# Optimization experiments

Measured on AMD Instinct MI355X. Metric: run time of the kernel, lower is better.

## Reference

```python
import jax, jax.numpy as jnp
import numpy as np

B, L, D, F_, H = 64, 64, 512, 32, 512  # batch, seq_len, in_dim, fanout, hidden_dim


def setup_inputs() -> dict:
    key = jax.random.key(0)
    ks = jax.random.split(key, 8)
    x = jax.random.normal(ks[0], (B, L, D), dtype=jnp.float32)
    idx1 = jax.random.randint(ks[1], (B, F_), 0, L)          # hop-1 neighbor token ids
    idx2 = jax.random.randint(ks[2], (B, F_ * F_), 0, L)     # hop-2 neighbor token ids
    s_d = 1.0 / np.sqrt(D)
    s_h = 1.0 / np.sqrt(H)
    W_aggr0 = jax.random.normal(ks[3], (D, H), dtype=jnp.float32) * s_d
    b_aggr0 = jnp.zeros((H,), dtype=jnp.float32)
    W_self0 = jax.random.normal(ks[4], (D, H), dtype=jnp.float32) * s_d
    W_aggr1 = jax.random.normal(ks[5], (H, H), dtype=jnp.float32) * s_h
    b_aggr1 = jnp.zeros((H,), dtype=jnp.float32)
    W_self1 = jax.random.normal(ks[6], (H, H), dtype=jnp.float32) * s_h
    return {"x": x, "idx1": idx1, "idx2": idx2,
            "W_aggr0": W_aggr0, "b_aggr0": b_aggr0, "W_self0": W_self0,
            "W_aggr1": W_aggr1, "b_aggr1": b_aggr1, "W_self1": W_self1}


def _sage_gcn(src, nbr, W_aggr, b_aggr, W_self):
    # src: [B, N, d]; nbr: [B, N, F, d]. mean-aggregate + linear, sum with self-transform.
    aggr = jnp.mean(nbr, axis=2) @ W_aggr + b_aggr          # NeighborAggregator('mean')
    return src @ W_self + aggr                               # aggr_hidden_method='sum'


def reference(x, idx1, idx2, W_aggr0, b_aggr0, W_self0, W_aggr1, b_aggr1, W_self1):
    # Gather sampled node features per aspect (level 0 = aspect node itself, index 0).
    f0 = x[:, :1, :]                                               # [B, 1, D]
    f1 = jnp.take_along_axis(x, idx1[:, :, None], axis=1)          # [B, F, D]
    f2 = jnp.take_along_axis(x, idx2[:, :, None], axis=1)          # [B, F*F, D]

    # Layer 0 (shared gcn[0] weights across hops), leaky_relu activation.
    h0 = jax.nn.leaky_relu(_sage_gcn(f0, f1[:, None, :, :], W_aggr0, b_aggr0, W_self0))          # [B,1,H]
    h1 = jax.nn.leaky_relu(_sage_gcn(f1, f2.reshape(B, F_, F_, D), W_aggr0, b_aggr0, W_self0))   # [B,F,H]

    # Layer 1 (gcn[-1], activation=None).
    out = _sage_gcn(h0, h1[:, None, :, :], W_aggr1, b_aggr1, W_self1)                             # [B,1,H]
    return out
```

## Files before the change

kernel.cpp:

```cpp
#include <hip/hip_runtime.h>
#include <hip/hip_bf16.h>

#define B_ 64
#define L_ 64
#define D_ 512
#define F_ 32
#define H_ 512
#define M_ROWS 2048
#define M2 2112
#define KA 1024

typedef __attribute__((ext_vector_type(8))) short bf16x8;
typedef __attribute__((ext_vector_type(4))) float f32x4;

__device__ __forceinline__ float leaky(float v) { return v > 0.0f ? v : 0.01f * v; }

__device__ __forceinline__ unsigned short f2bf(float v) {
  unsigned int b = __float_as_uint(v);
  unsigned int r = b + 0x7FFF + ((b >> 16) & 1);
  return (unsigned short)(r >> 16);
}
__device__ __forceinline__ float bf2f(unsigned short h) {
  return __uint_as_float(((unsigned int)h) << 16);
}
__device__ __forceinline__ void cvt_store4(unsigned short* ph, unsigned short* pl, float4 v) {
  ushort4 h, l;
  h.x = f2bf(v.x); l.x = f2bf(v.x - bf2f(h.x));
  h.y = f2bf(v.y); l.y = f2bf(v.y - bf2f(h.y));
  h.z = f2bf(v.z); l.z = f2bf(v.z - bf2f(h.z));
  h.w = f2bf(v.w); l.w = f2bf(v.w - bf2f(h.w));
  *(ushort4*)ph = h;
  *(ushort4*)pl = l;
}

#define GLOAD16(GP, LP)                                              \
  __builtin_amdgcn_global_load_lds(                                  \
      (const __attribute__((address_space(1))) unsigned int*)(GP),   \
      (__attribute__((address_space(3))) unsigned int*)(LP), 16, 0, 0)

__global__ __launch_bounds__(256) void prep(
    const float* __restrict__ x, const int* __restrict__ idx1,
    const int* __restrict__ idx2,
    const float* __restrict__ Ws0, const float* __restrict__ Wa0,
    const float* __restrict__ Ws1, const float* __restrict__ Wa1,
    unsigned short* __restrict__ Xhi, unsigned short* __restrict__ Xlo,
    unsigned short* __restrict__ Mh, unsigned short* __restrict__ Ml,
    unsigned short* __restrict__ W0thi, unsigned short* __restrict__ W0tlo,
    unsigned short* __restrict__ W1thi, unsigned short* __restrict__ W1tlo) {
  __shared__ __align__(16) char smem[33024];
  const int blk = blockIdx.x;
  const int t = threadIdx.x;

  if (blk < 64) {
    const int b = blk;
    const float* src = x + (size_t)b * (L_ * D_);
    unsigned short* dh = Xhi + (size_t)b * (L_ * D_);
    unsigned short* dl = Xlo + (size_t)b * (L_ * D_);
#pragma unroll 4
    for (int i = 0; i < 32; ++i) {
      const int f4 = t + 256 * i;
      const float4 v = *(const float4*)(src + (size_t)f4 * 4);
      cvt_store4(dh + (size_t)f4 * 4, dl + (size_t)f4 * 4, v);
    }
  } else if (blk < 320) {
    const int q = blk - 64;
    const int k0 = (q & 15) * 64;
    const int n0 = ((q >> 4) & 7) * 64;
    const int cat = q >> 7;
    float (*lt)[72] = (float(*)[72])smem;
    const float* src = (cat == 0)
        ? (k0 < 512 ? Ws0 + (size_t)k0 * H_ : Wa0 + (size_t)(k0 - 512) * H_)
        : (k0 < 512 ? Ws1 + (size_t)k0 * H_ : Wa1 + (size_t)(k0 - 512) * H_);
    unsigned short* dhi = (cat == 0) ? W0thi : W1thi;
    unsigned short* dlo = (cat == 0) ? W0tlo : W1tlo;
#pragma unroll
    for (int i = 0; i < 4; ++i) {
      const int idx4 = t + 256 * i;
      const int kl = idx4 >> 4;
      const int n4 = (idx4 & 15) * 4;
      *(float4*)&lt[kl][n4] = *(const float4*)(src + (size_t)kl * H_ + n0 + n4);
    }
    __syncthreads();
#pragma unroll
    for (int i = 0; i < 4; ++i) {
      const int idx4 = t + 256 * i;
      const int nl = idx4 >> 4;
      const int k4 = (idx4 & 15) * 4;
      ushort4 h, l;
      const float v0 = lt[k4 + 0][nl], v1 = lt[k4 + 1][nl];
      const float v2 = lt[k4 + 2][nl], v3 = lt[k4 + 3][nl];
      h.x = f2bf(v0); l.x = f2bf(v0 - bf2f(h.x));
      h.y = f2bf(v1); l.y = f2bf(v1 - bf2f(h.y));
      h.z = f2bf(v2); l.z = f2bf(v2 - bf2f(h.z));
      h.w = f2bf(v3); l.w = f2bf(v3 - bf2f(h.w));
      *(ushort4*)(dhi + (size_t)(n0 + nl) * KA + k0 + k4) = h;
      *(ushort4*)(dlo + (size_t)(n0 + nl) * KA + k0 + k4) = l;
    }
  } else {
    const int q = blk - 320;
    const int b = q >> 2;
    const int nt0 = (q & 3) * 2;
    unsigned int* cnt = (unsigned int*)smem;
    unsigned short* Cm = (unsigned short*)(smem + 8448);
    unsigned short* XTh = (unsigned short*)(smem + 14592);
    unsigned short* XTl = XTh + 64 * 72;
    const int lane = t & 63;
    const int w = t >> 6;
    const int lr = lane & 15;
    const int kb8 = (lane >> 4) * 8;

#pragma unroll
    for (int i = 0; i < 9; ++i) { const int p = t + 256 * i; if (p < 2112) cnt[p] = 0u; }
#pragma unroll
    for (int i = 0; i < 12; ++i) Cm[t + 256 * i] = 0;
    __syncthreads();
#pragma unroll
    for (int i = 0; i < 4; ++i) {
      const int j = t + 256 * i;
      atomicAdd(&cnt[(j >> 5) * 64 + idx2[(size_t)b * 1024 + j]], 1u);
    }
    if (t < 32) atomicAdd(&cnt[32 * 64 + idx1[b * F_ + t]], 1u);
    __syncthreads();
#pragma unroll
    for (int i = 0; i < 9; ++i) {
      const int p = t + 256 * i;
      if (p < 2112) Cm[p] = f2bf((float)cnt[p] * 0.03125f);
    }
    __syncthreads();
    bf16x8 Af[3][2];
#pragma unroll
    for (int mi = 0; mi < 3; ++mi)
#pragma unroll
      for (int kt = 0; kt < 2; ++kt)
        Af[mi][kt] = *(const bf16x8*)&Cm[(mi * 16 + lr) * 64 + kt * 32 + kb8];

#pragma unroll
    for (int tt = 0; tt < 2; ++tt) {
      const int nbase = (nt0 + tt) * 64;
#pragma unroll
      for (int i = 0; i < 4; ++i) {
        const int f4 = t + 256 * i;
        const int l = f4 >> 4;
        const int c4 = (f4 & 15) * 4;
        const float4 v = *(const float4*)(x + (size_t)b * (L_ * D_) + (size_t)l * D_ + nbase + c4);
        unsigned short h;
        h = f2bf(v.x); XTh[(c4 + 0) * 72 + l] = h; XTl[(c4 + 0) * 72 + l] = f2bf(v.x - bf2f(h));
        h = f2bf(v.y); XTh[(c4 + 1) * 72 + l] = h; XTl[(c4 + 1) * 72 + l] = f2bf(v.y - bf2f(h));
        h = f2bf(v.z); XTh[(c4 + 2) * 72 + l] = h; XTl[(c4 + 2) * 72 + l] = f2bf(v.z - bf2f(h));
        h = f2bf(v.w); XTh[(c4 + 3) * 72 + l] = h; XTl[(c4 + 3) * 72 + l] = f2bf(v.w - bf2f(h));
      }
      __syncthreads();
      f32x4 acc[3] = {};
#pragma unroll
      for (int kt = 0; kt < 2; ++kt) {
        const bf16x8 Bh = *(const bf16x8*)&XTh[(w * 16 + lr) * 72 + kt * 32 + kb8];
        const bf16x8 Bl = *(const bf16x8*)&XTl[(w * 16 + lr) * 72 + kt * 32 + kb8];
#pragma unroll
        for (int mi = 0; mi < 3; ++mi) {
          acc[mi] = __builtin_amdgcn_mfma_f32_16x16x32_bf16(Af[mi][kt], Bh, acc[mi], 0, 0, 0);
          acc[mi] = __builtin_amdgcn_mfma_f32_16x16x32_bf16(Af[mi][kt], Bl, acc[mi], 0, 0, 0);
        }
      }
      const int col = nbase + w * 16 + lr;
#pragma unroll
      for (int mi = 0; mi < 3; ++mi)
#pragma unroll
        for (int r = 0; r < 4; ++r) {
          const int row48 = mi * 16 + (lane >> 4) * 4 + r;
          if (row48 > 32) continue;
          const size_t Mrow = (row48 < 32) ? (size_t)(b * F_ + row48) : (size_t)(M_ROWS + b);
          const float v = acc[mi][r];
          const unsigned short h = f2bf(v);
          Mh[Mrow * 512 + col] = h;
          Ml[Mrow * 512 + col] = f2bf(v - bf2f(h));
        }
      __syncthreads();
    }
  }
}

__global__ __launch_bounds__(256) void gemm1(
    const unsigned short* __restrict__ Xhi, const unsigned short* __restrict__ Xlo,
    const unsigned short* __restrict__ Mh, const unsigned short* __restrict__ Ml,
    const unsigned short* __restrict__ Wthi, const unsigned short* __restrict__ Wtlo,
    const int* __restrict__ idx1, const float* __restrict__ b0,
    unsigned short* __restrict__ Hhi, unsigned short* __restrict__ Hlo) {
  __shared__ unsigned short lds[24576];
  const int tid = threadIdx.x;
  const int lane = tid & 63;
  const int w = tid >> 6;
  const int wr = w >> 1, wc = w & 1;
  const int lr = lane & 15;
  const int kb = lane >> 4;
  const int swz = lr & 7;
  const int rsel = lane >> 3;
  const int cbs = ((lane & 7) ^ rsel) * 8;

  const int o = blockIdx.x;
  const int s = (o & 7) * 66 + (o >> 3);
  const int bmi = s >> 4;
  const int bni = s & 15;
  const int bm = bmi * 64;
  const int bn = bni * 32;

  int xrow[8];
  if (w < 2) {
#pragma unroll
    for (int i = 0; i < 8; ++i) {
      const int R = bm + rsel + 8 * i;
      if (bmi < 32) xrow[i] = (R >> 5) * 64 + idx1[R];
      else          xrow[i] = (R - M_ROWS) * 64;
    }
  }
  const unsigned short* Xp = (w == 0) ? Xhi : Xlo;
  const unsigned short* Mp = (w == 0) ? Mh : Ml;
  const unsigned short* Wp = (w == 2) ? Wthi : Wtlo;
  const unsigned short* mbase = Mp + (size_t)(bm + rsel) * 512 + cbs;
  const unsigned short* wbase = Wp + (size_t)(bn + rsel) * KA + cbs;
  const int PB = (w == 0) ? 0 : (w == 1) ? 4096 : (w == 2) ? 8192 : 10240;

#define STAGE(KT, BUF)                                                        \
  {                                                                           \
    unsigned short* ldst = &lds[(BUF)*12288 + PB];                            \
    if (w < 2) {                                                              \
      if ((KT) < 8) {                                                         \
        const int co = (KT)*64 + cbs;                                         \
        _Pragma("unroll") for (int i = 0; i < 8; ++i)                         \
            GLOAD16(Xp + (size_t)xrow[i] * 512 + co, ldst + i * 512);         \
      } else {                                                                \
        const unsigned short* mb = mbase + ((KT)-8) * 64;                     \
        _Pragma("unroll") for (int i = 0; i < 8; ++i)                         \
            GLOAD16(mb + (size_t)i * 8 * 512, ldst + i * 512);                \
      }                                                                       \
    } else {                                                                  \
      const unsigned short* wb = wbase + (KT)*64;                             \
      _Pragma("unroll") for (int i = 0; i < 4; ++i)                           \
          GLOAD16(wb + (size_t)i * 8 * KA, ldst + i * 512);                   \
    }                                                                         \
  }

  f32x4 acc[2] = {};
  STAGE(0, 0);
  __syncthreads();

#define AFRAG(PL, ROW, CB) \
  (*(const bf16x8*)&lds[buf * 12288 + (PL)*4096 + (ROW)*64 + (((CB) ^ swz) * 8)])
#define BFRAG(PL, ROW, CB) \
  (*(const bf16x8*)&lds[buf * 12288 + 8192 + (PL)*2048 + (ROW)*64 + (((CB) ^ swz) * 8)])

  for (int kt = 0; kt < 16; ++kt) {
    const int buf = kt & 1;
    if (kt < 15) STAGE(kt + 1, buf ^ 1);
#pragma unroll
    for (int ks = 0; ks < 2; ++ks) {
      const int c = ks * 4 + kb;
      const bf16x8 Ah0 = AFRAG(0, wr * 32 + lr, c);
      const bf16x8 Ah1 = AFRAG(0, wr * 32 + 16 + lr, c);
      const bf16x8 Al0 = AFRAG(1, wr * 32 + lr, c);
      const bf16x8 Al1 = AFRAG(1, wr * 32 + 16 + lr, c);
      const bf16x8 Bh = BFRAG(0, wc * 16 + lr, c);
      const bf16x8 Bl = BFRAG(1, wc * 16 + lr, c);
      acc[0] = __builtin_amdgcn_mfma_f32_16x16x32_bf16(Ah0, Bh, acc[0], 0, 0, 0);
      acc[0] = __builtin_amdgcn_mfma_f32_16x16x32_bf16(Ah0, Bl, acc[0], 0, 0, 0);
      acc[0] = __builtin_amdgcn_mfma_f32_16x16x32_bf16(Al0, Bh, acc[0], 0, 0, 0);
      acc[1] = __builtin_amdgcn_mfma_f32_16x16x32_bf16(Ah1, Bh, acc[1], 0, 0, 0);
      acc[1] = __builtin_amdgcn_mfma_f32_16x16x32_bf16(Ah1, Bl, acc[1], 0, 0, 0);
      acc[1] = __builtin_amdgcn_mfma_f32_16x16x32_bf16(Al1, Bh, acc[1], 0, 0, 0);
    }
    __syncthreads();
  }
#undef AFRAG
#undef BFRAG
#undef STAGE

  const int col = bn + wc * 16 + lr;
  const float bias = b0[col];
  if (bmi < 32) {
    const int b = bmi * 2 + wr;
    float sum = 0.f;
#pragma unroll
    for (int mi = 0; mi < 2; ++mi)
#pragma unroll
      for (int r = 0; r < 4; ++r) sum += leaky(acc[mi][r] + bias);
    sum += __shfl_xor(sum, 16);
    sum += __shfl_xor(sum, 32);
    sum *= (1.0f / 32.0f);
    if (lane < 16) {
      const unsigned short h = f2bf(sum);
      Hhi[(size_t)b * KA + 512 + col] = h;
      Hlo[(size_t)b * KA + 512 + col] = f2bf(sum - bf2f(h));
    }
  } else {
#pragma unroll
    for (int mi = 0; mi < 2; ++mi)
#pragma unroll
      for (int r = 0; r < 4; ++r) {
        const int b = wr * 32 + mi * 16 + kb * 4 + r;
        const float v = leaky(acc[mi][r] + bias);
        const unsigned short h = f2bf(v);
        Hhi[(size_t)b * KA + col] = h;
        Hlo[(size_t)b * KA + col] = f2bf(v - bf2f(h));
      }
  }
}

__global__ __launch_bounds__(256) void gemm2(
    const unsigned short* __restrict__ Hhi, const unsigned short* __restrict__ Hlo,
    const unsigned short* __restrict__ Wthi, const unsigned short* __restrict__ Wtlo,
    float* __restrict__ part) {
  __shared__ float sacc[256][17];
  const int tid = threadIdx.x;
  const int w = tid >> 6;
  const int lane = tid & 63;
  const int lr = lane & 15;
  const int kb = lane >> 4;
  const int n0 = blockIdx.x * 16;
  const int kc = blockIdx.y * 128;

  f32x4 acc[4] = {};
  const int k = kc + w * 32 + kb * 8;
  const bf16x8 Bh = *(const bf16x8*)(Wthi + (size_t)(n0 + lr) * KA + k);
  const bf16x8 Bl = *(const bf16x8*)(Wtlo + (size_t)(n0 + lr) * KA + k);
#pragma unroll
  for (int mi = 0; mi < 4; ++mi) {
    const bf16x8 Ah = *(const bf16x8*)(Hhi + (size_t)(mi * 16 + lr) * KA + k);
    const bf16x8 Al = *(const bf16x8*)(Hlo + (size_t)(mi * 16 + lr) * KA + k);
    acc[mi] = __builtin_amdgcn_mfma_f32_16x16x32_bf16(Ah, Bh, acc[mi], 0, 0, 0);
    acc[mi] = __builtin_amdgcn_mfma_f32_16x16x32_bf16(Ah, Bl, acc[mi], 0, 0, 0);
    acc[mi] = __builtin_amdgcn_mfma_f32_16x16x32_bf16(Al, Bh, acc[mi], 0, 0, 0);
  }
#pragma unroll
  for (int mi = 0; mi < 4; ++mi)
#pragma unroll
    for (int r = 0; r < 4; ++r)
      sacc[((w * 4 + mi) * 4 + kb) * 4 + r][lr] = acc[mi][r];
  __syncthreads();

  const int lr2 = tid & 15;
  const int rg = tid >> 4;
  float* pp = part + (size_t)blockIdx.y * (B_ * H_);
#pragma unroll
  for (int q = 0; q < 4; ++q) {
    const int row = rg * 4 + q;
    const int mi = row >> 4, kb2 = (row >> 2) & 3, r = row & 3;
    float s = 0.f;
#pragma unroll
    for (int w2 = 0; w2 < 4; ++w2)
      s += sacc[((w2 * 4 + mi) * 4 + kb2) * 4 + r][lr2];
    pp[(size_t)row * H_ + n0 + lr2] = s;
  }
}

__global__ __launch_bounds__(256) void reduce_out(
    const float* __restrict__ part, const float* __restrict__ b1,
    float* __restrict__ out) {
  const int idx = blockIdx.x * 256 + threadIdx.x;
  const int c4 = (idx & 127) * 4;
  const size_t off = (size_t)(idx >> 7) * H_ + c4;
  float4 s = *(const float4*)(b1 + c4);
#pragma unroll
  for (int ky = 0; ky < 8; ++ky) {
    const float4 p = *(const float4*)(part + (size_t)ky * (B_ * H_) + off);
    s.x += p.x; s.y += p.y; s.z += p.z; s.w += p.w;
  }
  *(float4*)(out + off) = s;
}

extern "C" void kernel_launch(void* const* d_in, const int* in_sizes, int n_in,
                              void* d_out, int out_size, void* d_ws, size_t ws_size,
                              hipStream_t stream) {
  const float* x    = (const float*)d_in[0];
  const int*   idx1 = (const int*)d_in[1];
  const int*   idx2 = (const int*)d_in[2];
  const float* Wa0  = (const float*)d_in[3];
  const float* b0   = (const float*)d_in[4];
  const float* Ws0  = (const float*)d_in[5];
  const float* Wa1  = (const float*)d_in[6];
  const float* b1   = (const float*)d_in[7];
  const float* Ws1  = (const float*)d_in[8];
  float* out = (float*)d_out;

  unsigned short* wsu = (unsigned short*)d_ws;
  unsigned short* Xhi   = wsu;
  unsigned short* Xlo   = Xhi + (size_t)4096 * 512;
  unsigned short* Mh    = Xlo + (size_t)4096 * 512;
  unsigned short* Ml    = Mh + (size_t)M2 * 512;
  unsigned short* W0thi = Ml + (size_t)M2 * 512;
  unsigned short* W0tlo = W0thi + (size_t)H_ * KA;
  unsigned short* W1thi = W0tlo + (size_t)H_ * KA;
  unsigned short* W1tlo = W1thi + (size_t)H_ * KA;
  unsigned short* Hhi   = W1tlo + (size_t)H_ * KA;
  unsigned short* Hlo   = Hhi + (size_t)B_ * KA;
  float* part = (float*)(Hlo + (size_t)B_ * KA);

  prep<<<576, 256, 0, stream>>>(x, idx1, idx2, Ws0, Wa0, Ws1, Wa1,
                                Xhi, Xlo, Mh, Ml, W0thi, W0tlo, W1thi, W1tlo);
  gemm1<<<528, 256, 0, stream>>>(Xhi, Xlo, Mh, Ml, W0thi, W0tlo,
                                 idx1, b0, Hhi, Hlo);
  gemm2<<<dim3(32, 8), 256, 0, stream>>>(Hhi, Hlo, W1thi, W1tlo, part);
  reduce_out<<<32, 256, 0, stream>>>(part, b1, out);
}
```

Measured before the change: 40.64 us.

## Apply layer-0 weights before neighbor aggregation and fuse count-matrix mean into GEMM

Layer 0 now multiplies all 64 tokens per batch by the concatenated self and aggregate weights first. It then builds the neighbor means by multiplying the bf16 count matrix with the projected result inside one fused kernel. This removes the separate pre-aggregation pass that wrote the M matrices and the gather-indexed GEMM. The price is a kernel without double buffering, a larger per-block output tile, and more LDS reuse in the epilogue.

```diff
diff --git a/kernel.cpp b/kernel.cpp
--- a/kernel.cpp
+++ b/kernel.cpp
@@ -6,9 +6,6 @@
 #define D_ 512
 #define F_ 32
 #define H_ 512
-#define M_ROWS 2048
-#define M2 2112
-#define KA 1024
 
 typedef __attribute__((ext_vector_type(8))) short bf16x8;
 typedef __attribute__((ext_vector_type(4))) float f32x4;
@@ -44,10 +41,10 @@
     const float* __restrict__ Ws0, const float* __restrict__ Wa0,
     const float* __restrict__ Ws1, const float* __restrict__ Wa1,
     unsigned short* __restrict__ Xhi, unsigned short* __restrict__ Xlo,
-    unsigned short* __restrict__ Mh, unsigned short* __restrict__ Ml,
     unsigned short* __restrict__ W0thi, unsigned short* __restrict__ W0tlo,
-    unsigned short* __restrict__ W1thi, unsigned short* __restrict__ W1tlo) {
-  __shared__ __align__(16) char smem[33024];
+    unsigned short* __restrict__ W1thi, unsigned short* __restrict__ W1tlo,
+    unsigned short* __restrict__ Cm) {
+  __shared__ __align__(16) char smem[18432 + 2304];
   const int blk = blockIdx.x;
   const int t = threadIdx.x;
 
@@ -63,22 +60,39 @@
       cvt_store4(dh + (size_t)f4 * 4, dl + (size_t)f4 * 4, v);
     }
   } else if (blk < 320) {
-    const int q = blk - 64;
-    const int k0 = (q & 15) * 64;
-    const int n0 = ((q >> 4) & 7) * 64;
-    const int cat = q >> 7;
     float (*lt)[72] = (float(*)[72])smem;
-    const float* src = (cat == 0)
-        ? (k0 < 512 ? Ws0 + (size_t)k0 * H_ : Wa0 + (size_t)(k0 - 512) * H_)
-        : (k0 < 512 ? Ws1 + (size_t)k0 * H_ : Wa1 + (size_t)(k0 - 512) * H_);
-    unsigned short* dhi = (cat == 0) ? W0thi : W1thi;
-    unsigned short* dlo = (cat == 0) ? W0tlo : W1tlo;
-#pragma unroll
-    for (int i = 0; i < 4; ++i) {
-      const int idx4 = t + 256 * i;
-      const int kl = idx4 >> 4;
-      const int n4 = (idx4 & 15) * 4;
-      *(float4*)&lt[kl][n4] = *(const float4*)(src + (size_t)kl * H_ + n0 + n4);
+    const float* src;
+    unsigned short *dhi, *dlo;
+    int k0, n0, ncol0, dstride;
+    if (blk < 192) {
+      const int q = blk - 64;
+      k0 = (q & 7) * 64;
+      n0 = (q >> 3) * 64;
+      if (n0 < 512) { src = Ws0; ncol0 = n0; } else { src = Wa0; ncol0 = n0 - 512; }
+      dhi = W0thi; dlo = W0tlo; dstride = 512;
+    } else {
+      const int q = blk - 192;
+      k0 = (q & 15) * 64;
+      n0 = (q >> 4) * 64;
+      if (k0 < 512) { src = Ws1 + (size_t)k0 * H_; } else { src = Wa1 + (size_t)(k0 - 512) * H_; }
+      ncol0 = n0; k0 = (blk - 192 & 15) * 64; dhi = W1thi; dlo = W1tlo; dstride = 1024;
+    }
+    if (blk < 192) {
+#pragma unroll
+      for (int i = 0; i < 4; ++i) {
+        const int idx4 = t + 256 * i;
+        const int kl = idx4 >> 4;
+        const int n4 = (idx4 & 15) * 4;
+        *(float4*)&lt[kl][n4] = *(const float4*)(src + (size_t)(k0 + kl) * H_ + ncol0 + n4);
+      }
+    } else {
+#pragma unroll
+      for (int i = 0; i < 4; ++i) {
+        const int idx4 = t + 256 * i;
+        const int kl = idx4 >> 4;
+        const int n4 = (idx4 & 15) * 4;
+        *(float4*)&lt[kl][n4] = *(const float4*)(src + (size_t)kl * H_ + ncol0 + n4);
+      }
     }
     __syncthreads();
 #pragma unroll
@@ -93,26 +107,14 @@
       h.y = f2bf(v1); l.y = f2bf(v1 - bf2f(h.y));
       h.z = f2bf(v2); l.z = f2bf(v2 - bf2f(h.z));
       h.w = f2bf(v3); l.w = f2bf(v3 - bf2f(h.w));
-      *(ushort4*)(dhi + (size_t)(n0 + nl) * KA + k0 + k4) = h;
-      *(ushort4*)(dlo + (size_t)(n0 + nl) * KA + k0 + k4) = l;
+      *(ushort4*)(dhi + (size_t)(n0 + nl) * dstride + k0 + k4) = h;
+      *(ushort4*)(dlo + (size_t)(n0 + nl) * dstride + k0 + k4) = l;
     }
   } else {
-    const int q = blk - 320;
-    const int b = q >> 2;
-    const int nt0 = (q & 3) * 2;
+    const int b = blk - 320;
     unsigned int* cnt = (unsigned int*)smem;
-    unsigned short* Cm = (unsigned short*)(smem + 8448);
-    unsigned short* XTh = (unsigned short*)(smem + 14592);
-    unsigned short* XTl = XTh + 64 * 72;
-    const int lane = t & 63;
-    const int w = t >> 6;
-    const int lr = lane & 15;
-    const int kb8 = (lane >> 4) * 8;
-
 #pragma unroll
     for (int i = 0; i < 9; ++i) { const int p = t + 256 * i; if (p < 2112) cnt[p] = 0u; }
-#pragma unroll
-    for (int i = 0; i < 12; ++i) Cm[t + 256 * i] = 0;
     __syncthreads();
 #pragma unroll
     for (int i = 0; i < 4; ++i) {
@@ -122,185 +124,163 @@
     if (t < 32) atomicAdd(&cnt[32 * 64 + idx1[b * F_ + t]], 1u);
     __syncthreads();
 #pragma unroll
-    for (int i = 0; i < 9; ++i) {
+    for (int i = 0; i < 12; ++i) {
       const int p = t + 256 * i;
-      if (p < 2112) Cm[p] = f2bf((float)cnt[p] * 0.03125f);
-    }
-    __syncthreads();
-    bf16x8 Af[3][2];
-#pragma unroll
-    for (int mi = 0; mi < 3; ++mi)
-#pragma unroll
-      for (int kt = 0; kt < 2; ++kt)
-        Af[mi][kt] = *(const bf16x8*)&Cm[(mi * 16 + lr) * 64 + kt * 32 + kb8];
-
-#pragma unroll
-    for (int tt = 0; tt < 2; ++tt) {
-      const int nbase = (nt0 + tt) * 64;
-#pragma unroll
-      for (int i = 0; i < 4; ++i) {
-        const int f4 = t + 256 * i;
-        const int l = f4 >> 4;
-        const int c4 = (f4 & 15) * 4;
-        const float4 v = *(const float4*)(x + (size_t)b * (L_ * D_) + (size_t)l * D_ + nbase + c4);
-        unsigned short h;
-        h = f2bf(v.x); XTh[(c4 + 0) * 72 + l] = h; XTl[(c4 + 0) * 72 + l] = f2bf(v.x - bf2f(h));
-        h = f2bf(v.y); XTh[(c4 + 1) * 72 + l] = h; XTl[(c4 + 1) * 72 + l] = f2bf(v.y - bf2f(h));
-        h = f2bf(v.z); XTh[(c4 + 2) * 72 + l] = h; XTl[(c4 + 2) * 72 + l] = f2bf(v.z - bf2f(h));
-        h = f2bf(v.w); XTh[(c4 + 3) * 72 + l] = h; XTl[(c4 + 3) * 72 + l] = f2bf(v.w - bf2f(h));
-      }
-      __syncthreads();
-      f32x4 acc[3] = {};
-#pragma unroll
-      for (int kt = 0; kt < 2; ++kt) {
-        const bf16x8 Bh = *(const bf16x8*)&XTh[(w * 16 + lr) * 72 + kt * 32 + kb8];
-        const bf16x8 Bl = *(const bf16x8*)&XTl[(w * 16 + lr) * 72 + kt * 32 + kb8];
-#pragma unroll
-        for (int mi = 0; mi < 3; ++mi) {
-          acc[mi] = __builtin_amdgcn_mfma_f32_16x16x32_bf16(Af[mi][kt], Bh, acc[mi], 0, 0, 0);
-          acc[mi] = __builtin_amdgcn_mfma_f32_16x16x32_bf16(Af[mi][kt], Bl, acc[mi], 0, 0, 0);
-        }
-      }
-      const int col = nbase + w * 16 + lr;
-#pragma unroll
-      for (int mi = 0; mi < 3; ++mi)
-#pragma unroll
-        for (int r = 0; r < 4; ++r) {
-          const int row48 = mi * 16 + (lane >> 4) * 4 + r;
-          if (row48 > 32) continue;
-          const size_t Mrow = (row48 < 32) ? (size_t)(b * F_ + row48) : (size_t)(M_ROWS + b);
-          const float v = acc[mi][r];
-          const unsigned short h = f2bf(v);
-          Mh[Mrow * 512 + col] = h;
-          Ml[Mrow * 512 + col] = f2bf(v - bf2f(h));
-        }
-      __syncthreads();
-    }
-  }
-}
-
-__global__ __launch_bounds__(256) void gemm1(
+      Cm[(size_t)b * 3072 + p] = (p < 2112) ? f2bf((float)cnt[p] * 0.03125f) : (unsigned short)0;
+    }
+  }
+}
+
+__global__ __launch_bounds__(256) void fused1(
     const unsigned short* __restrict__ Xhi, const unsigned short* __restrict__ Xlo,
-    const unsigned short* __restrict__ Mh, const unsigned short* __restrict__ Ml,
-    const unsigned short* __restrict__ Wthi, const unsigned short* __restrict__ Wtlo,
-    const int* __restrict__ idx1, const float* __restrict__ b0,
-    unsigned short* __restrict__ Hhi, unsigned short* __restrict__ Hlo) {
-  __shared__ unsigned short lds[24576];
+    const unsigned short* __restrict__ W0thi, const unsigned short* __restrict__ W0tlo,
+    const unsigned short* __restrict__ Cm, const int* __restrict__ idx1,
+    const float* __restrict__ b0, unsigned short* __restrict__ Hhi,
+    unsigned short* __restrict__ Hlo) {
+  __shared__ __align__(16) unsigned short lds[24576];
   const int tid = threadIdx.x;
   const int lane = tid & 63;
   const int w = tid >> 6;
   const int wr = w >> 1, wc = w & 1;
   const int lr = lane & 15;
   const int kb = lane >> 4;
-  const int swz = lr & 7;
-  const int rsel = lane >> 3;
-  const int cbs = ((lane & 7) ^ rsel) * 8;
+  const int rl = lane >> 3;
+  const int cbs = ((lane & 7) ^ rl) * 8;
 
   const int o = blockIdx.x;
-  const int s = (o & 7) * 66 + (o >> 3);
-  const int bmi = s >> 4;
-  const int bni = s & 15;
-  const int bm = bmi * 64;
-  const int bn = bni * 32;
-
-  int xrow[8];
-  if (w < 2) {
-#pragma unroll
-    for (int i = 0; i < 8; ++i) {
-      const int R = bm + rsel + 8 * i;
-      if (bmi < 32) xrow[i] = (R >> 5) * 64 + idx1[R];
-      else          xrow[i] = (R - M_ROWS) * 64;
-    }
-  }
-  const unsigned short* Xp = (w == 0) ? Xhi : Xlo;
-  const unsigned short* Mp = (w == 0) ? Mh : Ml;
-  const unsigned short* Wp = (w == 2) ? Wthi : Wtlo;
-  const unsigned short* mbase = Mp + (size_t)(bm + rsel) * 512 + cbs;
-  const unsigned short* wbase = Wp + (size_t)(bn + rsel) * KA + cbs;
-  const int PB = (w == 0) ? 0 : (w == 1) ? 4096 : (w == 2) ? 8192 : 10240;
-
-#define STAGE(KT, BUF)                                                        \
-  {                                                                           \
-    unsigned short* ldst = &lds[(BUF)*12288 + PB];                            \
-    if (w < 2) {                                                              \
-      if ((KT) < 8) {                                                         \
-        const int co = (KT)*64 + cbs;                                         \
-        _Pragma("unroll") for (int i = 0; i < 8; ++i)                         \
-            GLOAD16(Xp + (size_t)xrow[i] * 512 + co, ldst + i * 512);         \
-      } else {                                                                \
-        const unsigned short* mb = mbase + ((KT)-8) * 64;                     \
-        _Pragma("unroll") for (int i = 0; i < 8; ++i)                         \
-            GLOAD16(mb + (size_t)i * 8 * 512, ldst + i * 512);                \
-      }                                                                       \
-    } else {                                                                  \
-      const unsigned short* wb = wbase + (KT)*64;                             \
-      _Pragma("unroll") for (int i = 0; i < 4; ++i)                           \
-          GLOAD16(wb + (size_t)i * 8 * KA, ldst + i * 512);                   \
-    }                                                                         \
-  }
-
-  f32x4 acc[2] = {};
-  STAGE(0, 0);
+  const int b = (o & 7) * 8 + (o >> 6);
+  const int s = (o >> 3) & 7;
+
+  f32x4 acc[2][4] = {};
+
+  for (int kt = 0; kt < 8; ++kt) {
+    const int kcol = kt * 64 + cbs;
+#pragma unroll
+    for (int i = 0; i < 12; ++i) {
+      const int slot = w * 12 + i;
+      const unsigned short* gp;
+      int ldsoff;
+      if (slot < 8) {
+        gp = Xhi + (size_t)(b * 64 + slot * 8 + rl) * 512 + kcol;
+        ldsoff = slot * 512;
+      } else if (slot < 16) {
+        const int u = slot - 8;
+        gp = Xlo + (size_t)(b * 64 + u * 8 + rl) * 512 + kcol;
+        ldsoff = 4096 + u * 512;
+      } else if (slot < 32) {
+        const int u = slot - 16;
+        const int row = (u >= 8 ? 512 : 0) + s * 64 + (u & 7) * 8 + rl;
+        gp = W0thi + (size_t)row * 512 + kcol;
+        ldsoff = 8192 + u * 512;
+      } else {
+        const int u = slot - 32;
+        const int row = (u >= 8 ? 512 : 0) + s * 64 + (u & 7) * 8 + rl;
+        gp = W0tlo + (size_t)row * 512 + kcol;
+        ldsoff = 16384 + u * 512;
+      }
+      GLOAD16(gp, &lds[ldsoff]);
+    }
+    __syncthreads();
+
+#define FRG(base, row, CB) \
+  (*(const bf16x8*)&lds[(base) + (row) * 64 + (((CB) ^ (lr & 7)) * 8)])
+#pragma unroll
+    for (int ks = 0; ks < 2; ++ks) {
+      const int CB = ks * 4 + kb;
+      const bf16x8 Ah0 = FRG(0, wr * 32 + lr, CB);
+      const bf16x8 Ah1 = FRG(0, wr * 32 + 16 + lr, CB);
+      const bf16x8 Al0 = FRG(4096, wr * 32 + lr, CB);
+      const bf16x8 Al1 = FRG(4096, wr * 32 + 16 + lr, CB);
+#pragma unroll
+      for (int ni = 0; ni < 4; ++ni) {
+        const int brow = wc * 64 + ni * 16 + lr;
+        const bf16x8 Bh = FRG(8192, brow, CB);
+        const bf16x8 Bl = FRG(16384, brow, CB);
+        acc[0][ni] = __builtin_amdgcn_mfma_f32_16x16x32_bf16(Ah0, Bh, acc[0][ni], 0, 0, 0);
+        acc[0][ni] = __builtin_amdgcn_mfma_f32_16x16x32_bf16(Ah0, Bl, acc[0][ni], 0, 0, 0);
+        acc[0][ni] = __builtin_amdgcn_mfma_f32_16x16x32_bf16(Al0, Bh, acc[0][ni], 0, 0, 0);
+        acc[1][ni] = __builtin_amdgcn_mfma_f32_16x16x32_bf16(Ah1, Bh, acc[1][ni], 0, 0, 0);
+        acc[1][ni] = __builtin_amdgcn_mfma_f32_16x16x32_bf16(Ah1, Bl, acc[1][ni], 0, 0, 0);
+        acc[1][ni] = __builtin_amdgcn_mfma_f32_16x16x32_bf16(Al1, Bh, acc[1][ni], 0, 0, 0);
+      }
+    }
+#undef FRG
+    __syncthreads();
+  }
+
+  float* Ysf = (float*)lds;
+  unsigned short* Yh = (unsigned short*)((char*)lds + 17408);
+  unsigned short* Yl = Yh + 64 * 72;
+
+  if (wc == 0) {
+#pragma unroll
+    for (int mi = 0; mi < 2; ++mi)
+#pragma unroll
+      for (int ni = 0; ni < 4; ++ni)
+#pragma unroll
+        for (int r = 0; r < 4; ++r) {
+          const int row = wr * 32 + mi * 16 + kb * 4 + r;
+          const int c = ni * 16 + lr;
+          Ysf[row * 68 + c] = acc[mi][ni][r];
+        }
+  } else {
+#pragma unroll
+    for (int mi = 0; mi < 2; ++mi)
+#pragma unroll
+      for (int ni = 0; ni < 4; ++ni)
+#pragma unroll
+        for (int r = 0; r < 4; ++r) {
+          const int row = wr * 32 + mi * 16 + kb * 4 + r;
+          const int c = ni * 16 + lr;
+          const float v = acc[mi][ni][r];
+          const unsigned short h = f2bf(v);
+          Yh[c * 72 + row] = h;
+          Yl[c * 72 + row] = f2bf(v - bf2f(h));
+        }
+  }
   __syncthreads();
 
-#define AFRAG(PL, ROW, CB) \
-  (*(const bf16x8*)&lds[buf * 12288 + (PL)*4096 + (ROW)*64 + (((CB) ^ swz) * 8)])
-#define BFRAG(PL, ROW, CB) \
-  (*(const bf16x8*)&lds[buf * 12288 + 8192 + (PL)*2048 + (ROW)*64 + (((CB) ^ swz) * 8)])
-
-  for (int kt = 0; kt < 16; ++kt) {
-    const int buf = kt & 1;
-    if (kt < 15) STAGE(kt + 1, buf ^ 1);
-#pragma unroll
-    for (int ks = 0; ks < 2; ++ks) {
-      const int c = ks * 4 + kb;
-      const bf16x8 Ah0 = AFRAG(0, wr * 32 + lr, c);
-      const bf16x8 Ah1 = AFRAG(0, wr * 32 + 16 + lr, c);
-      const bf16x8 Al0 = AFRAG(1, wr * 32 + lr, c);
-      const bf16x8 Al1 = AFRAG(1, wr * 32 + 16 + lr, c);
-      const bf16x8 Bh = BFRAG(0, wc * 16 + lr, c);
-      const bf16x8 Bl = BFRAG(1, wc * 16 + lr, c);
-      acc[0] = __builtin_amdgcn_mfma_f32_16x16x32_bf16(Ah0, Bh, acc[0], 0, 0, 0);
-      acc[0] = __builtin_amdgcn_mfma_f32_16x16x32_bf16(Ah0, Bl, acc[0], 0, 0, 0);
-      acc[0] = __builtin_amdgcn_mfma_f32_16x16x32_bf16(Al0, Bh, acc[0], 0, 0, 0);
-      acc[1] = __builtin_amdgcn_mfma_f32_16x16x32_bf16(Ah1, Bh, acc[1], 0, 0, 0);
-      acc[1] = __builtin_amdgcn_mfma_f32_16x16x32_bf16(Ah1, Bl, acc[1], 0, 0, 0);
-      acc[1] = __builtin_amdgcn_mfma_f32_16x16x32_bf16(Al1, Bh, acc[1], 0, 0, 0);
-    }
-    __syncthreads();
-  }
-#undef AFRAG
-#undef BFRAG
-#undef STAGE
-
-  const int col = bn + wc * 16 + lr;
-  const float bias = b0[col];
-  if (bmi < 32) {
-    const int b = bmi * 2 + wr;
-    float sum = 0.f;
-#pragma unroll
-    for (int mi = 0; mi < 2; ++mi)
-#pragma unroll
-      for (int r = 0; r < 4; ++r) sum += leaky(acc[mi][r] + bias);
-    sum += __shfl_xor(sum, 16);
-    sum += __shfl_xor(sum, 32);
-    sum *= (1.0f / 32.0f);
-    if (lane < 16) {
-      const unsigned short h = f2bf(sum);
-      Hhi[(size_t)b * KA + 512 + col] = h;
-      Hlo[(size_t)b * KA + 512 + col] = f2bf(sum - bf2f(h));
-    }
-  } else {
-#pragma unroll
-    for (int mi = 0; mi < 2; ++mi)
-#pragma unroll
-      for (int r = 0; r < 4; ++r) {
-        const int b = wr * 32 + mi * 16 + kb * 4 + r;
-        const float v = leaky(acc[mi][r] + bias);
-        const unsigned short h = f2bf(v);
-        Hhi[(size_t)b * KA + col] = h;
-        Hlo[(size_t)b * KA + col] = f2bf(v - bf2f(h));
-      }
+  bf16x8 Af[3][2];
+#pragma unroll
+  for (int mi = 0; mi < 3; ++mi)
+#pragma unroll
+    for (int kf = 0; kf < 2; ++kf)
+      Af[mi][kf] = *(const bf16x8*)(Cm + (size_t)b * 3072 + (mi * 16 + lr) * 64 + kf * 32 + kb * 8);
+
+  f32x4 macc[3] = {};
+#pragma unroll
+  for (int kf = 0; kf < 2; ++kf) {
+    const bf16x8 Bh8 = *(const bf16x8*)&Yh[(w * 16 + lr) * 72 + kf * 32 + kb * 8];
+    const bf16x8 Bl8 = *(const bf16x8*)&Yl[(w * 16 + lr) * 72 + kf * 32 + kb * 8];
+#pragma unroll
+    for (int mi = 0; mi < 3; ++mi) {
+      macc[mi] = __builtin_amdgcn_mfma_f32_16x16x32_bf16(Af[mi][kf], Bh8, macc[mi], 0, 0, 0);
+      macc[mi] = __builtin_amdgcn_mfma_f32_16x16x32_bf16(Af[mi][kf], Bl8, macc[mi], 0, 0, 0);
+    }
+  }
+
+  const int c = w * 16 + lr;
+  const float bias = b0[s * 64 + c];
+  float sum = 0.f;
+#pragma unroll
+  for (int mi = 0; mi < 2; ++mi)
+#pragma unroll
+    for (int r = 0; r < 4; ++r) {
+      const int f = mi * 16 + kb * 4 + r;
+      const int xr = idx1[b * F_ + f];
+      sum += leaky(Ysf[xr * 68 + c] + macc[mi][r] + bias);
+    }
+  sum += __shfl_xor(sum, 16);
+  sum += __shfl_xor(sum, 32);
+  sum *= (1.0f / 32.0f);
+  if (lane < 16) {
+    unsigned short h = f2bf(sum);
+    Hhi[(size_t)b * 1024 + 512 + s * 64 + c] = h;
+    Hlo[(size_t)b * 1024 + 512 + s * 64 + c] = f2bf(sum - bf2f(h));
+    const float v0 = leaky(Ysf[c] + macc[2][0] + bias);
+    const unsigned short h0h = f2bf(v0);
+    Hhi[(size_t)b * 1024 + s * 64 + c] = h0h;
+    Hlo[(size_t)b * 1024 + s * 64 + c] = f2bf(v0 - bf2f(h0h));
   }
 }
 
@@ -319,12 +299,12 @@
 
   f32x4 acc[4] = {};
   const int k = kc + w * 32 + kb * 8;
-  const bf16x8 Bh = *(const bf16x8*)(Wthi + (size_t)(n0 + lr) * KA + k);
-  const bf16x8 Bl = *(const bf16x8*)(Wtlo + (size_t)(n0 + lr) * KA + k);
+  const bf16x8 Bh = *(const bf16x8*)(Wthi + (size_t)(n0 + lr) * 1024 + k);
+  const bf16x8 Bl = *(const bf16x8*)(Wtlo + (size_t)(n0 + lr) * 1024 + k);
 #pragma unroll
   for (int mi = 0; mi < 4; ++mi) {
-    const bf16x8 Ah = *(const bf16x8*)(Hhi + (size_t)(mi * 16 + lr) * KA + k);
-    const bf16x8 Al = *(const bf16x8*)(Hlo + (size_t)(mi * 16 + lr) * KA + k);
+    const bf16x8 Ah = *(const bf16x8*)(Hhi + (size_t)(mi * 16 + lr) * 1024 + k);
+    const bf16x8 Al = *(const bf16x8*)(Hlo + (size_t)(mi * 16 + lr) * 1024 + k);
     acc[mi] = __builtin_amdgcn_mfma_f32_16x16x32_bf16(Ah, Bh, acc[mi], 0, 0, 0);
     acc[mi] = __builtin_amdgcn_mfma_f32_16x16x32_bf16(Ah, Bl, acc[mi], 0, 0, 0);
     acc[mi] = __builtin_amdgcn_mfma_f32_16x16x32_bf16(Al, Bh, acc[mi], 0, 0, 0);
@@ -383,20 +363,18 @@
   unsigned short* wsu = (unsigned short*)d_ws;
   unsigned short* Xhi   = wsu;
   unsigned short* Xlo   = Xhi + (size_t)4096 * 512;
-  unsigned short* Mh    = Xlo + (size_t)4096 * 512;
-  unsigned short* Ml    = Mh + (size_t)M2 * 512;
-  unsigned short* W0thi = Ml + (size_t)M2 * 512;
-  unsigned short* W0tlo = W0thi + (size_t)H_ * KA;
-  unsigned short* W1thi = W0tlo + (size_t)H_ * KA;
-  unsigned short* W1tlo = W1thi + (size_t)H_ * KA;
-  unsigned short* Hhi   = W1tlo + (size_t)H_ * KA;
-  unsigned short* Hlo   = Hhi + (size_t)B_ * KA;
-  float* part = (float*)(Hlo + (size_t)B_ * KA);
-
-  prep<<<576, 256, 0, stream>>>(x, idx1, idx2, Ws0, Wa0, Ws1, Wa1,
-                                Xhi, Xlo, Mh, Ml, W0thi, W0tlo, W1thi, W1tlo);
-  gemm1<<<528, 256, 0, stream>>>(Xhi, Xlo, Mh, Ml, W0thi, W0tlo,
-                                 idx1, b0, Hhi, Hlo);
+  unsigned short* W0thi = Xlo + (size_t)4096 * 512;
+  unsigned short* W0tlo = W0thi + (size_t)1024 * 512;
+  unsigned short* W1thi = W0tlo + (size_t)1024 * 512;
+  unsigned short* W1tlo = W1thi + (size_t)512 * 1024;
+  unsigned short* CmP   = W1tlo + (size_t)512 * 1024;
+  unsigned short* Hhi   = CmP + (size_t)64 * 3072;
+  unsigned short* Hlo   = Hhi + (size_t)B_ * 1024;
+  float* part = (float*)(Hlo + (size_t)B_ * 1024);
+
+  prep<<<384, 256, 0, stream>>>(x, idx1, idx2, Ws0, Wa0, Ws1, Wa1,
+                                Xhi, Xlo, W0thi, W0tlo, W1thi, W1tlo, CmP);
+  fused1<<<512, 256, 0, stream>>>(Xhi, Xlo, W0thi, W0tlo, CmP, idx1, b0, Hhi, Hlo);
   gemm2<<<dim3(32, 8), 256, 0, stream>>>(Hhi, Hlo, W1thi, W1tlo, part);
   reduce_out<<<32, 256, 0, stream>>>(part, b1, out);
 }
```

New measurement: 41.92 us. 1.03x slower.

## Fuse split-K reduction into gemm2, rebalance prep blocks, and relayout M buffer

Applied to the files above, without the earlier changes.

The second GEMM now does its full K reduction inside one 512-thread block, with eight waves combining their partial sums through shared memory and adding the bias. This removes the separate reduce_out launch and the round trip of partial sums through global memory. The prep kernel also splits the x conversion across 512 blocks, and each neighbour-mean block now covers 128 columns in a single pass. The M buffer moves to a per-batch 48-row layout, so gemm1 uses per-row offsets. In exchange gemm2 runs on only 32 blocks, and prep needs more shared memory per block.

```diff
diff --git a/kernel.cpp b/kernel.cpp
--- a/kernel.cpp
+++ b/kernel.cpp
@@ -7,7 +7,6 @@
 #define F_ 32
 #define H_ 512
 #define M_ROWS 2048
-#define M2 2112
 #define KA 1024
 
 typedef __attribute__((ext_vector_type(8))) short bf16x8;
@@ -44,33 +43,31 @@
     const float* __restrict__ Ws0, const float* __restrict__ Wa0,
     const float* __restrict__ Ws1, const float* __restrict__ Wa1,
     unsigned short* __restrict__ Xhi, unsigned short* __restrict__ Xlo,
-    unsigned short* __restrict__ Mh, unsigned short* __restrict__ Ml,
     unsigned short* __restrict__ W0thi, unsigned short* __restrict__ W0tlo,
-    unsigned short* __restrict__ W1thi, unsigned short* __restrict__ W1tlo) {
-  __shared__ __align__(16) char smem[33024];
+    unsigned short* __restrict__ W1thi, unsigned short* __restrict__ W1tlo,
+    unsigned short* __restrict__ Mh, unsigned short* __restrict__ Ml) {
+  __shared__ __align__(16) char smem[51456];
   const int blk = blockIdx.x;
   const int t = threadIdx.x;
 
-  if (blk < 64) {
-    const int b = blk;
-    const float* src = x + (size_t)b * (L_ * D_);
-    unsigned short* dh = Xhi + (size_t)b * (L_ * D_);
-    unsigned short* dl = Xlo + (size_t)b * (L_ * D_);
-#pragma unroll 4
-    for (int i = 0; i < 32; ++i) {
-      const int f4 = t + 256 * i;
-      const float4 v = *(const float4*)(src + (size_t)f4 * 4);
-      cvt_store4(dh + (size_t)f4 * 4, dl + (size_t)f4 * 4, v);
-    }
-  } else if (blk < 320) {
-    const int q = blk - 64;
-    const int k0 = (q & 15) * 64;
-    const int n0 = ((q >> 4) & 7) * 64;
+  if (blk < 512) {
+    const int base = blk * 256 + t;
+#pragma unroll
+    for (int i = 0; i < 4; ++i) {
+      const int f4 = base + i * 131072;
+      const float4 v = *(const float4*)(x + (size_t)f4 * 4);
+      cvt_store4(Xhi + (size_t)f4 * 4, Xlo + (size_t)f4 * 4, v);
+    }
+  } else if (blk < 768) {
+    float (*lt)[72] = (float(*)[72])smem;
+    const int q = blk - 512;
     const int cat = q >> 7;
-    float (*lt)[72] = (float(*)[72])smem;
+    const int qq = q & 127;
+    const int k0 = (qq & 15) * 64;
+    const int n0 = (qq >> 4) * 64;
     const float* src = (cat == 0)
-        ? (k0 < 512 ? Ws0 + (size_t)k0 * H_ : Wa0 + (size_t)(k0 - 512) * H_)
-        : (k0 < 512 ? Ws1 + (size_t)k0 * H_ : Wa1 + (size_t)(k0 - 512) * H_);
+        ? ((k0 < 512) ? Ws0 + (size_t)k0 * H_ : Wa0 + (size_t)(k0 - 512) * H_)
+        : ((k0 < 512) ? Ws1 + (size_t)k0 * H_ : Wa1 + (size_t)(k0 - 512) * H_);
     unsigned short* dhi = (cat == 0) ? W0thi : W1thi;
     unsigned short* dlo = (cat == 0) ? W0tlo : W1tlo;
 #pragma unroll
@@ -97,22 +94,20 @@
       *(ushort4*)(dlo + (size_t)(n0 + nl) * KA + k0 + k4) = l;
     }
   } else {
-    const int q = blk - 320;
+    const int q = blk - 768;
     const int b = q >> 2;
-    const int nt0 = (q & 3) * 2;
+    const int cc = q & 3;
     unsigned int* cnt = (unsigned int*)smem;
-    unsigned short* Cm = (unsigned short*)(smem + 8448);
+    unsigned short* Cbf = (unsigned short*)(smem + 8448);
     unsigned short* XTh = (unsigned short*)(smem + 14592);
-    unsigned short* XTl = XTh + 64 * 72;
+    unsigned short* XTl = (unsigned short*)(smem + 33024);
     const int lane = t & 63;
     const int w = t >> 6;
     const int lr = lane & 15;
-    const int kb8 = (lane >> 4) * 8;
+    const int kb = lane >> 4;
 
 #pragma unroll
     for (int i = 0; i < 9; ++i) { const int p = t + 256 * i; if (p < 2112) cnt[p] = 0u; }
-#pragma unroll
-    for (int i = 0; i < 12; ++i) Cm[t + 256 * i] = 0;
     __syncthreads();
 #pragma unroll
     for (int i = 0; i < 4; ++i) {
@@ -122,60 +117,54 @@
     if (t < 32) atomicAdd(&cnt[32 * 64 + idx1[b * F_ + t]], 1u);
     __syncthreads();
 #pragma unroll
-    for (int i = 0; i < 9; ++i) {
+    for (int i = 0; i < 12; ++i) {
       const int p = t + 256 * i;
-      if (p < 2112) Cm[p] = f2bf((float)cnt[p] * 0.03125f);
-    }
-    __syncthreads();
-    bf16x8 Af[3][2];
-#pragma unroll
-    for (int mi = 0; mi < 3; ++mi)
-#pragma unroll
-      for (int kt = 0; kt < 2; ++kt)
-        Af[mi][kt] = *(const bf16x8*)&Cm[(mi * 16 + lr) * 64 + kt * 32 + kb8];
-
-#pragma unroll
-    for (int tt = 0; tt < 2; ++tt) {
-      const int nbase = (nt0 + tt) * 64;
-#pragma unroll
-      for (int i = 0; i < 4; ++i) {
-        const int f4 = t + 256 * i;
-        const int l = f4 >> 4;
-        const int c4 = (f4 & 15) * 4;
-        const float4 v = *(const float4*)(x + (size_t)b * (L_ * D_) + (size_t)l * D_ + nbase + c4);
-        unsigned short h;
-        h = f2bf(v.x); XTh[(c4 + 0) * 72 + l] = h; XTl[(c4 + 0) * 72 + l] = f2bf(v.x - bf2f(h));
-        h = f2bf(v.y); XTh[(c4 + 1) * 72 + l] = h; XTl[(c4 + 1) * 72 + l] = f2bf(v.y - bf2f(h));
-        h = f2bf(v.z); XTh[(c4 + 2) * 72 + l] = h; XTl[(c4 + 2) * 72 + l] = f2bf(v.z - bf2f(h));
-        h = f2bf(v.w); XTh[(c4 + 3) * 72 + l] = h; XTl[(c4 + 3) * 72 + l] = f2bf(v.w - bf2f(h));
-      }
-      __syncthreads();
-      f32x4 acc[3] = {};
-#pragma unroll
-      for (int kt = 0; kt < 2; ++kt) {
-        const bf16x8 Bh = *(const bf16x8*)&XTh[(w * 16 + lr) * 72 + kt * 32 + kb8];
-        const bf16x8 Bl = *(const bf16x8*)&XTl[(w * 16 + lr) * 72 + kt * 32 + kb8];
+      Cbf[p] = (p < 2112) ? f2bf((float)cnt[p] * 0.03125f) : (unsigned short)0;
+    }
+#pragma unroll
+    for (int i = 0; i < 8; ++i) {
+      const int idx4 = t + 256 * i;
+      const int l = idx4 >> 5;
+      const int c4 = (idx4 & 31) * 4;
+      const float4 v = *(const float4*)(x + (size_t)b * (L_ * D_) + (size_t)l * D_ + cc * 128 + c4);
+      unsigned short h;
+      h = f2bf(v.x); XTh[(c4 + 0) * 72 + l] = h; XTl[(c4 + 0) * 72 + l] = f2bf(v.x - bf2f(h));
+      h = f2bf(v.y); XTh[(c4 + 1) * 72 + l] = h; XTl[(c4 + 1) * 72 + l] = f2bf(v.y - bf2f(h));
+      h = f2bf(v.z); XTh[(c4 + 2) * 72 + l] = h; XTl[(c4 + 2) * 72 + l] = f2bf(v.z - bf2f(h));
+      h = f2bf(v.w); XTh[(c4 + 3) * 72 + l] = h; XTl[(c4 + 3) * 72 + l] = f2bf(v.w - bf2f(h));
+    }
+    __syncthreads();
+
+    f32x4 acc[3][2] = {};
+#pragma unroll
+    for (int kf = 0; kf < 2; ++kf) {
+#pragma unroll
+      for (int ni = 0; ni < 2; ++ni) {
+        const int coll = w * 32 + ni * 16 + lr;
+        const bf16x8 Bh = *(const bf16x8*)&XTh[coll * 72 + kf * 32 + kb * 8];
+        const bf16x8 Bl = *(const bf16x8*)&XTl[coll * 72 + kf * 32 + kb * 8];
 #pragma unroll
         for (int mi = 0; mi < 3; ++mi) {
-          acc[mi] = __builtin_amdgcn_mfma_f32_16x16x32_bf16(Af[mi][kt], Bh, acc[mi], 0, 0, 0);
-          acc[mi] = __builtin_amdgcn_mfma_f32_16x16x32_bf16(Af[mi][kt], Bl, acc[mi], 0, 0, 0);
+          const bf16x8 Af = *(const bf16x8*)&Cbf[(mi * 16 + lr) * 64 + kf * 32 + kb * 8];
+          acc[mi][ni] = __builtin_amdgcn_mfma_f32_16x16x32_bf16(Af, Bh, acc[mi][ni], 0, 0, 0);
+          acc[mi][ni] = __builtin_amdgcn_mfma_f32_16x16x32_bf16(Af, Bl, acc[mi][ni], 0, 0, 0);
         }
       }
-      const int col = nbase + w * 16 + lr;
-#pragma unroll
-      for (int mi = 0; mi < 3; ++mi)
+    }
+#pragma unroll
+    for (int mi = 0; mi < 3; ++mi)
+#pragma unroll
+      for (int ni = 0; ni < 2; ++ni)
 #pragma unroll
         for (int r = 0; r < 4; ++r) {
-          const int row48 = mi * 16 + (lane >> 4) * 4 + r;
+          const int row48 = mi * 16 + kb * 4 + r;
           if (row48 > 32) continue;
-          const size_t Mrow = (row48 < 32) ? (size_t)(b * F_ + row48) : (size_t)(M_ROWS + b);
-          const float v = acc[mi][r];
+          const int col = cc * 128 + w * 32 + ni * 16 + lr;
+          const float v = acc[mi][ni][r];
           const unsigned short h = f2bf(v);
-          Mh[Mrow * 512 + col] = h;
-          Ml[Mrow * 512 + col] = f2bf(v - bf2f(h));
+          Mh[((size_t)b * 48 + row48) * 512 + col] = h;
+          Ml[((size_t)b * 48 + row48) * 512 + col] = f2bf(v - bf2f(h));
         }
-      __syncthreads();
-    }
   }
 }
 
@@ -203,19 +192,24 @@
   const int bm = bmi * 64;
   const int bn = bni * 32;
 
-  int xrow[8];
+  int xrow[8], mrow[8];
   if (w < 2) {
 #pragma unroll
     for (int i = 0; i < 8; ++i) {
       const int R = bm + rsel + 8 * i;
-      if (bmi < 32) xrow[i] = (R >> 5) * 64 + idx1[R];
-      else          xrow[i] = (R - M_ROWS) * 64;
+      if (bmi < 32) {
+        xrow[i] = (R >> 5) * 64 + idx1[R];
+        mrow[i] = (R >> 5) * 48 + (R & 31);
+      } else {
+        const int bb = R - M_ROWS;
+        xrow[i] = bb * 64;
+        mrow[i] = bb * 48 + 32;
+      }
     }
   }
   const unsigned short* Xp = (w == 0) ? Xhi : Xlo;
   const unsigned short* Mp = (w == 0) ? Mh : Ml;
   const unsigned short* Wp = (w == 2) ? Wthi : Wtlo;
-  const unsigned short* mbase = Mp + (size_t)(bm + rsel) * 512 + cbs;
   const unsigned short* wbase = Wp + (size_t)(bn + rsel) * KA + cbs;
   const int PB = (w == 0) ? 0 : (w == 1) ? 4096 : (w == 2) ? 8192 : 10240;
 
@@ -228,9 +222,9 @@
         _Pragma("unroll") for (int i = 0; i < 8; ++i)                         \
             GLOAD16(Xp + (size_t)xrow[i] * 512 + co, ldst + i * 512);         \
       } else {                                                                \
-        const unsigned short* mb = mbase + ((KT)-8) * 64;                     \
+        const int co = ((KT)-8) * 64 + cbs;                                   \
         _Pragma("unroll") for (int i = 0; i < 8; ++i)                         \
-            GLOAD16(mb + (size_t)i * 8 * 512, ldst + i * 512);                \
+            GLOAD16(Mp + (size_t)mrow[i] * 512 + co, ldst + i * 512);         \
       }                                                                       \
     } else {                                                                  \
       const unsigned short* wb = wbase + (KT)*64;                             \
@@ -304,66 +298,51 @@
   }
 }
 
-__global__ __launch_bounds__(256) void gemm2(
+__global__ __launch_bounds__(512) void gemm2f(
     const unsigned short* __restrict__ Hhi, const unsigned short* __restrict__ Hlo,
     const unsigned short* __restrict__ Wthi, const unsigned short* __restrict__ Wtlo,
-    float* __restrict__ part) {
-  __shared__ float sacc[256][17];
+    const float* __restrict__ b1, float* __restrict__ out) {
+  __shared__ float sacc[8][1088];
   const int tid = threadIdx.x;
   const int w = tid >> 6;
   const int lane = tid & 63;
   const int lr = lane & 15;
   const int kb = lane >> 4;
   const int n0 = blockIdx.x * 16;
-  const int kc = blockIdx.y * 128;
+  const int kc = w * 128;
 
   f32x4 acc[4] = {};
-  const int k = kc + w * 32 + kb * 8;
-  const bf16x8 Bh = *(const bf16x8*)(Wthi + (size_t)(n0 + lr) * KA + k);
-  const bf16x8 Bl = *(const bf16x8*)(Wtlo + (size_t)(n0 + lr) * KA + k);
-#pragma unroll
-  for (int mi = 0; mi < 4; ++mi) {
-    const bf16x8 Ah = *(const bf16x8*)(Hhi + (size_t)(mi * 16 + lr) * KA + k);
-    const bf16x8 Al = *(const bf16x8*)(Hlo + (size_t)(mi * 16 + lr) * KA + k);
-    acc[mi] = __builtin_amdgcn_mfma_f32_16x16x32_bf16(Ah, Bh, acc[mi], 0, 0, 0);
-    acc[mi] = __builtin_amdgcn_mfma_f32_16x16x32_bf16(Ah, Bl, acc[mi], 0, 0, 0);
-    acc[mi] = __builtin_amdgcn_mfma_f32_16x16x32_bf16(Al, Bh, acc[mi], 0, 0, 0);
+#pragma unroll
+  for (int ks = 0; ks < 4; ++ks) {
+    const int k = kc + ks * 32 + kb * 8;
+    const bf16x8 Bh = *(const bf16x8*)(Wthi + (size_t)(n0 + lr) * KA + k);
+    const bf16x8 Bl = *(const bf16x8*)(Wtlo + (size_t)(n0 + lr) * KA + k);
+#pragma unroll
+    for (int mi = 0; mi < 4; ++mi) {
+      const bf16x8 Ah = *(const bf16x8*)(Hhi + (size_t)(mi * 16 + lr) * KA + k);
+      const bf16x8 Al = *(const bf16x8*)(Hlo + (size_t)(mi * 16 + lr) * KA + k);
+      acc[mi] = __builtin_amdgcn_mfma_f32_16x16x32_bf16(Ah, Bh, acc[mi], 0, 0, 0);
+      acc[mi] = __builtin_amdgcn_mfma_f32_16x16x32_bf16(Ah, Bl, acc[mi], 0, 0, 0);
+      acc[mi] = __builtin_amdgcn_mfma_f32_16x16x32_bf16(Al, Bh, acc[mi], 0, 0, 0);
+    }
   }
 #pragma unroll
   for (int mi = 0; mi < 4; ++mi)
 #pragma unroll
     for (int r = 0; r < 4; ++r)
-      sacc[((w * 4 + mi) * 4 + kb) * 4 + r][lr] = acc[mi][r];
+      sacc[w][(mi * 16 + kb * 4 + r) * 17 + lr] = acc[mi][r];
   __syncthreads();
 
-  const int lr2 = tid & 15;
-  const int rg = tid >> 4;
-  float* pp = part + (size_t)blockIdx.y * (B_ * H_);
-#pragma unroll
-  for (int q = 0; q < 4; ++q) {
-    const int row = rg * 4 + q;
-    const int mi = row >> 4, kb2 = (row >> 2) & 3, r = row & 3;
-    float s = 0.f;
-#pragma unroll
-    for (int w2 = 0; w2 < 4; ++w2)
-      s += sacc[((w2 * 4 + mi) * 4 + kb2) * 4 + r][lr2];
-    pp[(size_t)row * H_ + n0 + lr2] = s;
-  }
-}
-
-__global__ __launch_bounds__(256) void reduce_out(
-    const float* __restrict__ part, const float* __restrict__ b1,
-    float* __restrict__ out) {
-  const int idx = blockIdx.x * 256 + threadIdx.x;
-  const int c4 = (idx & 127) * 4;
-  const size_t off = (size_t)(idx >> 7) * H_ + c4;
-  float4 s = *(const float4*)(b1 + c4);
-#pragma unroll
-  for (int ky = 0; ky < 8; ++ky) {
-    const float4 p = *(const float4*)(part + (size_t)ky * (B_ * H_) + off);
-    s.x += p.x; s.y += p.y; s.z += p.z; s.w += p.w;
-  }
-  *(float4*)(out + off) = s;
+#pragma unroll
+  for (int q = 0; q < 2; ++q) {
+    const int oid = tid * 2 + q;
+    const int row = oid >> 4;
+    const int col = oid & 15;
+    float sv = b1[n0 + col];
+#pragma unroll
+    for (int w2 = 0; w2 < 8; ++w2) sv += sacc[w2][row * 17 + col];
+    out[(size_t)row * H_ + n0 + col] = sv;
+  }
 }
 
 extern "C" void kernel_launch(void* const* d_in, const int* in_sizes, int n_in,
@@ -383,20 +362,18 @@
   unsigned short* wsu = (unsigned short*)d_ws;
   unsigned short* Xhi   = wsu;
   unsigned short* Xlo   = Xhi + (size_t)4096 * 512;
-  unsigned short* Mh    = Xlo + (size_t)4096 * 512;
-  unsigned short* Ml    = Mh + (size_t)M2 * 512;
-  unsigned short* W0thi = Ml + (size_t)M2 * 512;
+  unsigned short* W0thi = Xlo + (size_t)4096 * 512;
   unsigned short* W0tlo = W0thi + (size_t)H_ * KA;
   unsigned short* W1thi = W0tlo + (size_t)H_ * KA;
   unsigned short* W1tlo = W1thi + (size_t)H_ * KA;
-  unsigned short* Hhi   = W1tlo + (size_t)H_ * KA;
+  unsigned short* Mhp   = W1tlo + (size_t)H_ * KA;
+  unsigned short* Mlp   = Mhp + (size_t)64 * 48 * 512;
+  unsigned short* Hhi   = Mlp + (size_t)64 * 48 * 512;
   unsigned short* Hlo   = Hhi + (size_t)B_ * KA;
-  float* part = (float*)(Hlo + (size_t)B_ * KA);
-
-  prep<<<576, 256, 0, stream>>>(x, idx1, idx2, Ws0, Wa0, Ws1, Wa1,
-                                Xhi, Xlo, Mh, Ml, W0thi, W0tlo, W1thi, W1tlo);
-  gemm1<<<528, 256, 0, stream>>>(Xhi, Xlo, Mh, Ml, W0thi, W0tlo,
+
+  prep<<<1024, 256, 0, stream>>>(x, idx1, idx2, Ws0, Wa0, Ws1, Wa1,
+                                 Xhi, Xlo, W0thi, W0tlo, W1thi, W1tlo, Mhp, Mlp);
+  gemm1<<<528, 256, 0, stream>>>(Xhi, Xlo, Mhp, Mlp, W0thi, W0tlo,
                                  idx1, b0, Hhi, Hlo);
-  gemm2<<<dim3(32, 8), 256, 0, stream>>>(Hhi, Hlo, W1thi, W1tlo, part);
-  reduce_out<<<32, 256, 0, stream>>>(part, b1, out);
-}
+  gemm2f<<<32, 512, 0, stream>>>(Hhi, Hlo, W1thi, W1tlo, b1, out);
+}
```

New measurement: 47.46 us. +16.8%, slower.
